# Performance work log

Measured on AMD Instinct MI355X. Metric: run time of the kernel, lower is better.

Reference implementation:

```python
import jax, jax.numpy as jnp
import numpy as np

B, S, D_IN, D_OUT, H = 4, 2048, 768, 768, 12
DH = D_OUT // H


def setup_inputs() -> dict:
    key = jax.random.key(0)
    ks = jax.random.split(key, 6)
    x = jax.random.normal(ks[0], (B, S, D_IN), dtype=jnp.float32)
    # causal mask: True above the diagonal means "masked out" (filled with -inf)
    mask = jnp.triu(jnp.ones((S, S), dtype=bool), k=1)
    sc = 1.0 / np.sqrt(D_IN)
    Wq = jax.random.normal(ks[1], (D_IN, D_OUT), dtype=jnp.float32) * sc
    Wk = jax.random.normal(ks[2], (D_IN, D_OUT), dtype=jnp.float32) * sc
    Wv = jax.random.normal(ks[3], (D_IN, D_OUT), dtype=jnp.float32) * sc
    Wo = jax.random.normal(ks[4], (D_OUT, D_OUT), dtype=jnp.float32) * (1.0 / np.sqrt(D_OUT))
    bo = jnp.zeros((D_OUT,), dtype=jnp.float32)
    return {"input_tensor": x, "mask": mask, "Wq": Wq, "Wk": Wk, "Wv": Wv, "Wo": Wo, "bo": bo}


def reference(input_tensor, mask, Wq, Wk, Wv, Wo, bo):
    b, n, _ = input_tensor.shape
    # projections -> [b, h, n, dh]
    q = (input_tensor @ Wq).reshape(b, n, H, DH).transpose(0, 2, 1, 3)
    k = (input_tensor @ Wk).reshape(b, n, H, DH).transpose(0, 2, 1, 3)
    v = (input_tensor @ Wv).reshape(b, n, H, DH).transpose(0, 2, 1, 3)
    # scores [b, h, n, n]
    scores = jnp.einsum('bhqd,bhkd->bhqk', q, k)
    scores = jnp.where(mask[:n, :n], -jnp.inf, scores)
    attn = jax.nn.softmax(scores / np.sqrt(DH), axis=-1)
    ctx = jnp.einsum('bhqk,bhkd->bhqd', attn, v)
    ctx = ctx.transpose(0, 2, 1, 3).reshape(b, n, D_OUT)
    return ctx @ Wo + bo
```

## Files before the change

### kernel.cpp

```cpp
#include <hip/hip_runtime.h>
#include <hip/hip_bf16.h>
#include <math.h>

typedef __attribute__((ext_vector_type(4))) float f32x4;
typedef __attribute__((ext_vector_type(8))) short s16x8;
typedef __attribute__((ext_vector_type(8))) unsigned short u16x8;

#define B_ 4
#define S_ 2048
#define DIN 768
#define DOUT 768
#define H_ 12
#define DH_ 64
#define M_ (B_*S_)

__device__ __forceinline__ unsigned short f2bf(float f) {
  union { float f; unsigned u; } v; v.f = f;
  unsigned r = v.u + 0x7fffu + ((v.u >> 16) & 1u);
  return (unsigned short)(r >> 16);
}

#if __has_builtin(__builtin_amdgcn_exp2f)
#define EXP2(x) __builtin_amdgcn_exp2f(x)
#else
#define EXP2(x) exp2f(x)
#endif


__global__ __launch_bounds__(256) void prep(
    const float* __restrict__ X, unsigned short* __restrict__ Xb,
    const float* __restrict__ W0, const float* __restrict__ W1,
    const float* __restrict__ W2, const float* __restrict__ W3,
    unsigned short* __restrict__ Wt)
{
  __shared__ float t[32][33];
  const int bid = blockIdx.x;
  if (bid < 3072) {
    size_t i = ((size_t)bid * 256 + threadIdx.x) * 8;
    float4 a = *(const float4*)&X[i];
    float4 b = *(const float4*)&X[i + 4];
    u16x8 v;
    v[0] = f2bf(a.x); v[1] = f2bf(a.y); v[2] = f2bf(a.z); v[3] = f2bf(a.w);
    v[4] = f2bf(b.x); v[5] = f2bf(b.y); v[6] = f2bf(b.z); v[7] = f2bf(b.w);
    *(u16x8*)&Xb[i] = v;
  } else {
    const int t4 = bid - 3072;
    const int z = t4 / 576, rem = t4 - z * 576;
    const int ky = rem / 24, nx = rem - ky * 24;
    const float* W = z == 0 ? W0 : z == 1 ? W1 : z == 2 ? W2 : W3;
    unsigned short* Out = Wt + (size_t)z * DOUT * DIN;
    const int n0 = nx * 32, k0 = ky * 32;
    const int tx = threadIdx.x & 31, ty = threadIdx.x >> 5;
#pragma unroll
    for (int i = 0; i < 32; i += 8)
      t[ty + i][tx] = W[(size_t)(k0 + ty + i) * DOUT + n0 + tx];
    __syncthreads();
#pragma unroll
    for (int i = 0; i < 32; i += 8)
      Out[(size_t)(n0 + ty + i) * DIN + k0 + tx] = f2bf(t[tx][ty + i]);
  }
}


#define BKC 64
#define A_TILE_E (128 * BKC)
#define B_TILE_E (96 * BKC)

template <int OPS>
__device__ __forceinline__ void stage_tile(
    const unsigned short* __restrict__ g, int row0, int k0,
    unsigned short* lds, int tid)
{
#pragma unroll
  for (int it = 0; it < OPS; ++it) {
    int s = it * 256 + tid;
    int row = s >> 3, sc = s & 7;
    int gc = sc ^ (row & 7);
    const unsigned short* gsrc = g + (size_t)(row0 + row) * 768 + k0 + gc * 8;
    unsigned short* dst = lds + (size_t)(it * 256 + (tid & ~63)) * 8;
    __builtin_amdgcn_global_load_lds(
        (const __attribute__((address_space(1))) void*)gsrc,
        (__attribute__((address_space(3))) void*)dst, 16, 0, 0);
  }
}

__device__ __forceinline__ void gemm_core(
    const unsigned short* __restrict__ A, const unsigned short* __restrict__ Bt,
    int m0, int n0, unsigned short* As, unsigned short* Bs,
    f32x4 acc[4][3], int tid)
{
  const int lane = tid & 63;
  const int col_l = lane & 15, quad = lane >> 4;
  const int w = tid >> 6;
  const int wm = (w & 1) * 64, wn = (w >> 1) * 48;

  stage_tile<4>(A, m0, 0, As, tid);
  stage_tile<3>(Bt, n0, 0, Bs, tid);

#pragma unroll 2
  for (int k0 = 0; k0 < 768; k0 += BKC) {
    const int cur = (k0 >> 6) & 1;
    const unsigned short* Asb = As + cur * A_TILE_E;
    const unsigned short* Bsb = Bs + cur * B_TILE_E;
    if (k0 + BKC < 768) {
      stage_tile<4>(A, m0, k0 + BKC, As + (cur ^ 1) * A_TILE_E, tid);
      stage_tile<3>(Bt, n0, k0 + BKC, Bs + (cur ^ 1) * B_TILE_E, tid);
      asm volatile("s_waitcnt vmcnt(7)" ::: "memory");
    } else {
      asm volatile("s_waitcnt vmcnt(0)" ::: "memory");
    }
    __builtin_amdgcn_s_barrier();

#pragma unroll
    for (int kk = 0; kk < 2; ++kk) {
      s16x8 af[4], bf[3];
#pragma unroll
      for (int t = 0; t < 4; ++t) {
        int ar = wm + t * 16 + col_l;
        af[t] = *(const s16x8*)&Asb[ar * BKC + (((kk << 2) + quad) ^ (ar & 7)) * 8];
      }
#pragma unroll
      for (int t = 0; t < 3; ++t) {
        int br = wn + t * 16 + col_l;
        bf[t] = *(const s16x8*)&Bsb[br * BKC + (((kk << 2) + quad) ^ (br & 7)) * 8];
      }
#pragma unroll
      for (int mt = 0; mt < 4; ++mt)
#pragma unroll
        for (int nt = 0; nt < 3; ++nt)
          acc[mt][nt] = __builtin_amdgcn_mfma_f32_16x16x32_bf16(
              af[mt], bf[nt], acc[mt][nt], 0, 0, 0);
    }

    __builtin_amdgcn_s_barrier();
  }
}

__global__ __launch_bounds__(256) void proj_mfma(
    const unsigned short* __restrict__ Xb, const unsigned short* __restrict__ Wt,
    unsigned short* __restrict__ Qo, unsigned short* __restrict__ Ko,
    unsigned short* __restrict__ Vo)
{
  __shared__ unsigned short As[2 * A_TILE_E];
  __shared__ unsigned short Bs[2 * B_TILE_E];
  const int tid = threadIdx.x;

  const int orig = (blockIdx.z * 64 + blockIdx.y) * 8 + blockIdx.x;
  const int id = (orig & 7) * 192 + (orig >> 3);
  const int z = id / 512;
  const int r = id - z * 512;
  const int my = r >> 3, nx = r & 7;
  const int m0 = my * 128, n0 = nx * 96;

  const unsigned short* Bw = Wt + (size_t)z * DOUT * DIN;
  unsigned short* Out = z == 0 ? Qo : z == 1 ? Ko : Vo;
  const float scale = z == 0 ? 0.125f * 1.44269504f : 1.0f;

  f32x4 acc[4][3] = {};
  gemm_core(Xb, Bw, m0, n0, As, Bs, acc, tid);

  const int lane = tid & 63, w = tid >> 6;
  const int col_l = lane & 15, quad = lane >> 4;
  const int wm = (w & 1) * 64, wn = (w >> 1) * 48;
  if (z == 2) {
    const int mblk = m0 + wm;
    const int b = mblk >> 11, sblk = mblk & (S_ - 1);
#pragma unroll
    for (int mt = 0; mt < 4; ++mt) {
      const int slot = (mt >> 1) * 32 + quad * 8 + (mt & 1) * 4;
#pragma unroll
      for (int nt = 0; nt < 3; ++nt) {
        int n = n0 + wn + nt * 16 + col_l;
        int h = n >> 6, d = n & 63;
        ushort4 v;
        v.x = f2bf(acc[mt][nt][0]); v.y = f2bf(acc[mt][nt][1]);
        v.z = f2bf(acc[mt][nt][2]); v.w = f2bf(acc[mt][nt][3]);
        *(ushort4*)&Out[((size_t)(b * H_ + h) * DH_ + d) * S_ + sblk + slot] = v;
      }
    }
  } else {
#pragma unroll
    for (int mt = 0; mt < 4; ++mt)
#pragma unroll
      for (int nt = 0; nt < 3; ++nt) {
        int n = n0 + wn + nt * 16 + col_l;
        int h = n >> 6, d = n & 63;
#pragma unroll
        for (int r2 = 0; r2 < 4; ++r2) {
          int m = m0 + wm + mt * 16 + quad * 4 + r2;
          int b = m >> 11, s = m & (S_ - 1);
          Out[((size_t)(b * H_ + h) * S_ + s) * DH_ + d] = f2bf(acc[mt][nt][r2] * scale);
        }
      }
  }
}

__global__ __launch_bounds__(256) void out_mfma(
    const unsigned short* __restrict__ Cb, const unsigned short* __restrict__ Wt,
    const float* __restrict__ bo, float* __restrict__ Out)
{
  __shared__ unsigned short As[2 * A_TILE_E];
  __shared__ unsigned short Bs[2 * B_TILE_E];
  const int tid = threadIdx.x;

  const int orig = blockIdx.y * 8 + blockIdx.x;
  const int id = (orig & 7) * 64 + (orig >> 3);
  const int my = id >> 3, nx = id & 7;
  const int m0 = my * 128, n0 = nx * 96;

  f32x4 acc[4][3] = {};
  gemm_core(Cb, Wt, m0, n0, As, Bs, acc, tid);

  const int lane = tid & 63, w = tid >> 6;
  const int col_l = lane & 15, quad = lane >> 4;
  const int wm = (w & 1) * 64, wn = (w >> 1) * 48;
#pragma unroll
  for (int mt = 0; mt < 4; ++mt)
#pragma unroll
    for (int nt = 0; nt < 3; ++nt) {
      int n = n0 + wn + nt * 16 + col_l;
      float bias = bo[n];
#pragma unroll
      for (int r = 0; r < 4; ++r) {
        int m = m0 + wm + mt * 16 + quad * 4 + r;
        Out[(size_t)m * DOUT + n] = acc[mt][nt][r] + bias;
      }
    }
}


union PK { uint2 u2[2]; s16x8 v; };

#define MFMA_BF16 __builtin_amdgcn_mfma_f32_16x16x32_bf16

__device__ __forceinline__ void exppack(const f32x4 sc[4], PK& p0, PK& p1) {
#pragma unroll
  for (int nc = 0; nc < 4; ++nc) {
    float e0 = EXP2(sc[nc][0] - 17.3123405f);
    float e1 = EXP2(sc[nc][1] - 17.3123405f);
    float e2 = EXP2(sc[nc][2] - 17.3123405f);
    float e3 = EXP2(sc[nc][3] - 17.3123405f);
    union { __hip_bfloat162 v; unsigned u; } lo, hi;
    lo.v = __float22bfloat162_rn(make_float2(e0, e1));
    hi.v = __float22bfloat162_rn(make_float2(e2, e3));
    uint2 pw; pw.x = lo.u; pw.y = hi.u;
    if (nc < 2) p0.u2[nc] = pw; else p1.u2[nc - 2] = pw;
  }
}

__global__ __launch_bounds__(256, 3) void attn_mfma(
    const unsigned short* __restrict__ Q, const unsigned short* __restrict__ K,
    const unsigned short* __restrict__ Vt, unsigned short* __restrict__ CTX)
{
  __shared__ unsigned short Ks[2][64 * 64];
  __shared__ unsigned short Vs[2][64 * 64];

  const int tid = threadIdx.x;
  const int lane = tid & 63;
  const int w = tid >> 6;
  const int col_l = lane & 15;
  const int quad = lane >> 4;

  const int orig = (blockIdx.z * 12 + blockIdx.y) * 16 + blockIdx.x;
  const int id = (orig & 7) * 96 + (orig >> 3);
  const int p = id & 15;
  const int bh = id >> 4;
  const int h = bh % 12, b = bh / 12;

  const int q0A = p << 6, q0B = (31 - p) << 6;
  const int ntiles = 32 - p;
  const size_t bhs = (size_t)(b * H_ + h);
  const unsigned short* Qg = Q + bhs * S_ * DH_;
  const unsigned short* Kg = K + bhs * S_ * DH_;
  const unsigned short* Vg = Vt + bhs * DH_ * S_;

  const int qwA = q0A + (w << 4), qwB = q0B + (w << 4);
  s16x8 aqA0 = *(const s16x8*)&Qg[(size_t)(qwA + col_l) * DH_ + quad * 8];
  s16x8 aqA1 = *(const s16x8*)&Qg[(size_t)(qwA + col_l) * DH_ + 32 + quad * 8];
  s16x8 aqB0 = *(const s16x8*)&Qg[(size_t)(qwB + col_l) * DH_ + quad * 8];
  s16x8 aqB1 = *(const s16x8*)&Qg[(size_t)(qwB + col_l) * DH_ + 32 + quad * 8];

  const int krow = lane;
  const int kc0 = (w ^ (krow & 7)) * 8;
  const int kc1 = ((w + 4) ^ (krow & 7)) * 8;
  const int vrow = tid >> 3;
  const int vslot = tid & 7;
  const int vc = (vslot ^ (vrow & 7)) * 8;

  s16x8 kp0 = *(const s16x8*)&Kg[(size_t)krow * DH_ + w * 8];
  s16x8 kp1 = *(const s16x8*)&Kg[(size_t)krow * DH_ + (w + 4) * 8];
  s16x8 vp0 = *(const s16x8*)&Vg[(size_t)vrow * S_ + vslot * 8];
  s16x8 vp1 = *(const s16x8*)&Vg[(size_t)(vrow + 32) * S_ + vslot * 8];

  f32x4 oA[4] = {}, oB[4] = {}, lA = {}, lB = {};
  s16x8 bones;
#pragma unroll
  for (int i = 0; i < 8; ++i) bones[i] = (short)0x3F80;

  const int qrel = (w << 4) + col_l;
  const int r7 = col_l & 7;

  for (int t = 0; t < ntiles; ++t) {
    unsigned short* KsB = &Ks[t & 1][0];
    unsigned short* VsB = &Vs[t & 1][0];
    *(s16x8*)&KsB[krow * 64 + kc0] = kp0;
    *(s16x8*)&KsB[krow * 64 + kc1] = kp1;
    *(s16x8*)&VsB[vrow * 64 + vc] = vp0;
    *(s16x8*)&VsB[(vrow + 32) * 64 + vc] = vp1;
    __syncthreads();
    {
      const int jn = (t + 1 < ntiles ? t + 1 : t) << 6;
      kp0 = *(const s16x8*)&Kg[(size_t)(jn + krow) * DH_ + w * 8];
      kp1 = *(const s16x8*)&Kg[(size_t)(jn + krow) * DH_ + (w + 4) * 8];
      vp0 = *(const s16x8*)&Vg[(size_t)vrow * S_ + jn + vslot * 8];
      vp1 = *(const s16x8*)&Vg[(size_t)(vrow + 32) * S_ + jn + vslot * 8];
    }
    const bool doA = (t <= p);

    f32x4 scA[4], scB[4];
    __builtin_amdgcn_s_setprio(1);
#pragma unroll
    for (int nc = 0; nc < 4; ++nc) {
      const int kr = nc * 16 + col_l;
      s16x8 k0 = *(const s16x8*)&KsB[kr * 64 + ((quad ^ r7) * 8)];
      s16x8 k1 = *(const s16x8*)&KsB[kr * 64 + (((quad + 4) ^ r7) * 8)];
      f32x4 a = {};
      a = MFMA_BF16(k0, aqB0, a, 0, 0, 0);
      a = MFMA_BF16(k1, aqB1, a, 0, 0, 0);
      scB[nc] = a;
      if (doA) {
        f32x4 c = {};
        c = MFMA_BF16(k0, aqA0, c, 0, 0, 0);
        c = MFMA_BF16(k1, aqA1, c, 0, 0, 0);
        scA[nc] = c;
      }
    }
    __builtin_amdgcn_s_setprio(0);
    if (t == p) {
#pragma unroll
      for (int nc = 0; nc < 4; ++nc)
#pragma unroll
        for (int r = 0; r < 4; ++r)
          if (nc * 16 + quad * 4 + r > qrel) scA[nc][r] = -INFINITY;
    }
    if (t == ntiles - 1) {
#pragma unroll
      for (int nc = 0; nc < 4; ++nc)
#pragma unroll
        for (int r = 0; r < 4; ++r)
          if (nc * 16 + quad * 4 + r > qrel) scB[nc][r] = -INFINITY;
    }

    PK pA0, pA1, pB0, pB1;
    if (doA) exppack(scA, pA0, pA1);
    exppack(scB, pB0, pB1);

    __builtin_amdgcn_s_setprio(1);
#pragma unroll
    for (int dc = 0; dc < 4; ++dc) {
      const int vr = dc * 16 + col_l;
      s16x8 b0 = *(const s16x8*)&VsB[vr * 64 + ((quad ^ r7) * 8)];
      s16x8 b1 = *(const s16x8*)&VsB[vr * 64 + (((quad + 4) ^ r7) * 8)];
      oB[dc] = MFMA_BF16(pB0.v, b0, oB[dc], 0, 0, 0);
      oB[dc] = MFMA_BF16(pB1.v, b1, oB[dc], 0, 0, 0);
      if (doA) {
        oA[dc] = MFMA_BF16(pA0.v, b0, oA[dc], 0, 0, 0);
        oA[dc] = MFMA_BF16(pA1.v, b1, oA[dc], 0, 0, 0);
      }
    }
    lB = MFMA_BF16(pB0.v, bones, lB, 0, 0, 0);
    lB = MFMA_BF16(pB1.v, bones, lB, 0, 0, 0);
    if (doA) {
      lA = MFMA_BF16(pA0.v, bones, lA, 0, 0, 0);
      lA = MFMA_BF16(pA1.v, bones, lA, 0, 0, 0);
    }
    __builtin_amdgcn_s_setprio(0);
  }

  float liA[4], liB[4];
#pragma unroll
  for (int r = 0; r < 4; ++r) {
    liA[r] = 1.0f / lA[r];
    liB[r] = 1.0f / lB[r];
  }
#pragma unroll
  for (int dc = 0; dc < 4; ++dc)
#pragma unroll
    for (int r = 0; r < 4; ++r) {
      CTX[((size_t)(b * S_ + qwA + quad * 4 + r)) * DOUT + h * DH_ + dc * 16 + col_l]
          = f2bf(oA[dc][r] * liA[r]);
      CTX[((size_t)(b * S_ + qwB + quad * 4 + r)) * DOUT + h * DH_ + dc * 16 + col_l]
          = f2bf(oB[dc][r] * liB[r]);
    }
}


extern "C" void kernel_launch(void* const* d_in, const int* in_sizes, int n_in,
                              void* d_out, int out_size, void* d_ws, size_t ws_size,
                              hipStream_t stream) {
  const float* X  = (const float*)d_in[0];
  const float* Wq = (const float*)d_in[2];
  const float* Wk = (const float*)d_in[3];
  const float* Wv = (const float*)d_in[4];
  const float* Wo = (const float*)d_in[5];
  const float* bo = (const float*)d_in[6];
  float* out = (float*)d_out;

  unsigned short* Xb = (unsigned short*)d_ws;
  unsigned short* Wt = Xb + (size_t)M_ * DIN;
  unsigned short* Qb = Wt + (size_t)4 * DOUT * DIN;
  unsigned short* Kb = Qb + (size_t)M_ * DOUT;
  unsigned short* Vb = Kb + (size_t)M_ * DOUT;
  unsigned short* Cb = Vb + (size_t)M_ * DOUT;

  prep<<<dim3(3072 + 2304), 256, 0, stream>>>(X, Xb, Wq, Wk, Wv, Wo, Wt);
  proj_mfma<<<dim3(8, M_ / 128, 3), 256, 0, stream>>>(Xb, Wt, Qb, Kb, Vb);
  attn_mfma<<<dim3(16, H_, B_), 256, 0, stream>>>(Qb, Kb, Vb, Cb);
  out_mfma<<<dim3(8, M_ / 128), 256, 0, stream>>>(
      Cb, Wt + (size_t)3 * DOUT * DIN, bo, out);
}
```

Measured before the change: 195.2 us.

## Replace paired causal query tiles with one query tile per attention block

```diff
diff --git a/kernel.cpp b/kernel.cpp
--- a/kernel.cpp
+++ b/kernel.cpp
@@ -248,7 +248,7 @@
   }
 }
 
-__global__ __launch_bounds__(256, 3) void attn_mfma(
+__global__ __launch_bounds__(256, 5) void attn_mfma(
     const unsigned short* __restrict__ Q, const unsigned short* __restrict__ K,
     const unsigned short* __restrict__ Vt, unsigned short* __restrict__ CTX)
 {
@@ -261,24 +261,22 @@
   const int col_l = lane & 15;
   const int quad = lane >> 4;
 
-  const int orig = (blockIdx.z * 12 + blockIdx.y) * 16 + blockIdx.x;
-  const int id = (orig & 7) * 96 + (orig >> 3);
-  const int p = id & 15;
-  const int bh = id >> 4;
+  const int orig = (blockIdx.z * 12 + blockIdx.y) * 32 + blockIdx.x;
+  const int id = (orig & 7) * 192 + (orig >> 3);
+  const int q = id & 31;
+  const int bh = id >> 5;
   const int h = bh % 12, b = bh / 12;
 
-  const int q0A = p << 6, q0B = (31 - p) << 6;
-  const int ntiles = 32 - p;
+  const int q0 = q << 6;
+  const int ntiles = q + 1;
   const size_t bhs = (size_t)(b * H_ + h);
   const unsigned short* Qg = Q + bhs * S_ * DH_;
   const unsigned short* Kg = K + bhs * S_ * DH_;
   const unsigned short* Vg = Vt + bhs * DH_ * S_;
 
-  const int qwA = q0A + (w << 4), qwB = q0B + (w << 4);
-  s16x8 aqA0 = *(const s16x8*)&Qg[(size_t)(qwA + col_l) * DH_ + quad * 8];
-  s16x8 aqA1 = *(const s16x8*)&Qg[(size_t)(qwA + col_l) * DH_ + 32 + quad * 8];
-  s16x8 aqB0 = *(const s16x8*)&Qg[(size_t)(qwB + col_l) * DH_ + quad * 8];
-  s16x8 aqB1 = *(const s16x8*)&Qg[(size_t)(qwB + col_l) * DH_ + 32 + quad * 8];
+  const int qw = q0 + (w << 4);
+  s16x8 aq0 = *(const s16x8*)&Qg[(size_t)(qw + col_l) * DH_ + quad * 8];
+  s16x8 aq1 = *(const s16x8*)&Qg[(size_t)(qw + col_l) * DH_ + 32 + quad * 8];
 
   const int krow = lane;
   const int kc0 = (w ^ (krow & 7)) * 8;
@@ -292,7 +290,7 @@
   s16x8 vp0 = *(const s16x8*)&Vg[(size_t)vrow * S_ + vslot * 8];
   s16x8 vp1 = *(const s16x8*)&Vg[(size_t)(vrow + 32) * S_ + vslot * 8];
 
-  f32x4 oA[4] = {}, oB[4] = {}, lA = {}, lB = {};
+  f32x4 o[4] = {}, lacc = {};
   s16x8 bones;
 #pragma unroll
   for (int i = 0; i < 8; ++i) bones[i] = (short)0x3F80;
@@ -315,9 +313,8 @@
       vp0 = *(const s16x8*)&Vg[(size_t)vrow * S_ + jn + vslot * 8];
       vp1 = *(const s16x8*)&Vg[(size_t)(vrow + 32) * S_ + jn + vslot * 8];
     }
-    const bool doA = (t <= p);
-
-    f32x4 scA[4], scB[4];
+
+    f32x4 sc[4];
     __builtin_amdgcn_s_setprio(1);
 #pragma unroll
     for (int nc = 0; nc < 4; ++nc) {
@@ -325,35 +322,21 @@
       s16x8 k0 = *(const s16x8*)&KsB[kr * 64 + ((quad ^ r7) * 8)];
       s16x8 k1 = *(const s16x8*)&KsB[kr * 64 + (((quad + 4) ^ r7) * 8)];
       f32x4 a = {};
-      a = MFMA_BF16(k0, aqB0, a, 0, 0, 0);
-      a = MFMA_BF16(k1, aqB1, a, 0, 0, 0);
-      scB[nc] = a;
-      if (doA) {
-        f32x4 c = {};
-        c = MFMA_BF16(k0, aqA0, c, 0, 0, 0);
-        c = MFMA_BF16(k1, aqA1, c, 0, 0, 0);
-        scA[nc] = c;
-      }
+      a = MFMA_BF16(k0, aq0, a, 0, 0, 0);
+      a = MFMA_BF16(k1, aq1, a, 0, 0, 0);
+      sc[nc] = a;
     }
     __builtin_amdgcn_s_setprio(0);
-    if (t == p) {
+    if (t == ntiles - 1) {
 #pragma unroll
       for (int nc = 0; nc < 4; ++nc)
 #pragma unroll
         for (int r = 0; r < 4; ++r)
-          if (nc * 16 + quad * 4 + r > qrel) scA[nc][r] = -INFINITY;
-    }
-    if (t == ntiles - 1) {
-#pragma unroll
-      for (int nc = 0; nc < 4; ++nc)
-#pragma unroll
-        for (int r = 0; r < 4; ++r)
-          if (nc * 16 + quad * 4 + r > qrel) scB[nc][r] = -INFINITY;
-    }
-
-    PK pA0, pA1, pB0, pB1;
-    if (doA) exppack(scA, pA0, pA1);
-    exppack(scB, pB0, pB1);
+          if (nc * 16 + quad * 4 + r > qrel) sc[nc][r] = -INFINITY;
+    }
+
+    PK p0, p1;
+    exppack(sc, p0, p1);
 
     __builtin_amdgcn_s_setprio(1);
 #pragma unroll
@@ -361,37 +344,23 @@
       const int vr = dc * 16 + col_l;
       s16x8 b0 = *(const s16x8*)&VsB[vr * 64 + ((quad ^ r7) * 8)];
       s16x8 b1 = *(const s16x8*)&VsB[vr * 64 + (((quad + 4) ^ r7) * 8)];
-      oB[dc] = MFMA_BF16(pB0.v, b0, oB[dc], 0, 0, 0);
-      oB[dc] = MFMA_BF16(pB1.v, b1, oB[dc], 0, 0, 0);
-      if (doA) {
-        oA[dc] = MFMA_BF16(pA0.v, b0, oA[dc], 0, 0, 0);
-        oA[dc] = MFMA_BF16(pA1.v, b1, oA[dc], 0, 0, 0);
-      }
-    }
-    lB = MFMA_BF16(pB0.v, bones, lB, 0, 0, 0);
-    lB = MFMA_BF16(pB1.v, bones, lB, 0, 0, 0);
-    if (doA) {
-      lA = MFMA_BF16(pA0.v, bones, lA, 0, 0, 0);
-      lA = MFMA_BF16(pA1.v, bones, lA, 0, 0, 0);
-    }
+      o[dc] = MFMA_BF16(p0.v, b0, o[dc], 0, 0, 0);
+      o[dc] = MFMA_BF16(p1.v, b1, o[dc], 0, 0, 0);
+    }
+    lacc = MFMA_BF16(p0.v, bones, lacc, 0, 0, 0);
+    lacc = MFMA_BF16(p1.v, bones, lacc, 0, 0, 0);
     __builtin_amdgcn_s_setprio(0);
   }
 
-  float liA[4], liB[4];
-#pragma unroll
-  for (int r = 0; r < 4; ++r) {
-    liA[r] = 1.0f / lA[r];
-    liB[r] = 1.0f / lB[r];
-  }
+  float li[4];
+#pragma unroll
+  for (int r = 0; r < 4; ++r) li[r] = 1.0f / lacc[r];
 #pragma unroll
   for (int dc = 0; dc < 4; ++dc)
 #pragma unroll
-    for (int r = 0; r < 4; ++r) {
-      CTX[((size_t)(b * S_ + qwA + quad * 4 + r)) * DOUT + h * DH_ + dc * 16 + col_l]
-          = f2bf(oA[dc][r] * liA[r]);
-      CTX[((size_t)(b * S_ + qwB + quad * 4 + r)) * DOUT + h * DH_ + dc * 16 + col_l]
-          = f2bf(oB[dc][r] * liB[r]);
-    }
+    for (int r = 0; r < 4; ++r)
+      CTX[((size_t)(b * S_ + qw + quad * 4 + r)) * DOUT + h * DH_ + dc * 16 + col_l]
+          = f2bf(o[dc][r] * li[r]);
 }
 
 
@@ -415,7 +384,7 @@
 
   prep<<<dim3(3072 + 2304), 256, 0, stream>>>(X, Xb, Wq, Wk, Wv, Wo, Wt);
   proj_mfma<<<dim3(8, M_ / 128, 3), 256, 0, stream>>>(Xb, Wt, Qb, Kb, Vb);
-  attn_mfma<<<dim3(16, H_, B_), 256, 0, stream>>>(Qb, Kb, Vb, Cb);
+  attn_mfma<<<dim3(32, H_, B_), 256, 0, stream>>>(Qb, Kb, Vb, Cb);
   out_mfma<<<dim3(8, M_ / 128), 256, 0, stream>>>(
       Cb, Wt + (size_t)3 * DOUT * DIN, bo, out);
 }
```

Result: slower. 205.0 us (+5.1%).
